# Performance work log

Hardware: AMD Instinct MI355X
Metric: run time of the kernel (lower is better)

The kernel has to match this reference:

```python
import jax, jax.numpy as jnp
import numpy as np

B, D, M, H = 512, 2048, 32, 64  # batch, d_model, memory_length, memory_hidden_dims

def _glu(x):
    a, b = jnp.split(x, 2, axis=-1)
    return a * jax.nn.sigmoid(b)

def setup_inputs() -> dict:
    key = jax.random.key(0)
    k1, k2, k3 = jax.random.split(key, 3)
    s1 = 1.0 / np.sqrt(M + 2 * H)
    s2 = 1.0 / np.sqrt(H + 2)
    return {
        "state_trace": jax.random.normal(k1, (B, D, M), jnp.float32),
        "w1a": jax.random.uniform(k2, (M, 2 * H, D), jnp.float32, -s1, s1),
        "b1a": jnp.zeros((1, D, 2 * H), jnp.float32),
        "Ta": jnp.ones((1,), jnp.float32),
        "w1b": jax.random.uniform(k3, (H, 2, D), jnp.float32, -s2, s2),
        "b1b": jnp.zeros((1, D, 2), jnp.float32),
        "Tb": jnp.ones((1,), jnp.float32),
    }

def reference(state_trace, w1a, b1a, Ta, w1b, b1b, Tb):
    # SuperLinear 1: per-feature grouped matmul over d_model (D axis)
    x = (jnp.einsum('BDM,MHD->BDH', state_trace, w1a) + b1a) / Ta  # [B, D, 2H]
    x = _glu(x)                                                     # [B, D, H]
    # SuperLinear 2
    x = (jnp.einsum('BDM,MHD->BDH', x, w1b) + b1b) / Tb             # [B, D, 2]
    x = _glu(x)                                                     # [B, D, 1]
    return x.squeeze(-1)                                            # [B, D]
```

## Files before the change

### kernel.cpp

```cpp
#include <hip/hip_runtime.h>
#include <hip/hip_bf16.h>


#define NB 512
#define ND 2048
#define NM 32
#define NH2 128
#define DCHUNK 8
#define BTILE 64

typedef __bf16 bf16x8 __attribute__((ext_vector_type(8)));
typedef __bf16 bf16x4 __attribute__((ext_vector_type(4)));
typedef float f32x4 __attribute__((ext_vector_type(4)));
typedef float f32x2 __attribute__((ext_vector_type(2)));

#define WSA_BYTES ((size_t)ND * NH2 * NM * 2)

__device__ __forceinline__ float sigmoid_fast(float x) {
    return __builtin_amdgcn_rcpf(1.0f + __builtin_amdgcn_exp2f(-1.442695040888963f * x));
}

__global__ __launch_bounds__(256) void transpose_w(const float* __restrict__ w1a,
                                                   const float* __restrict__ w1b,
                                                   __bf16* __restrict__ wsA,
                                                   float* __restrict__ wsB) {
    __shared__ float tile[64 * 65];
    const int tid = threadIdx.x;
    if (blockIdx.x < 2048) {
        const int h0 = (blockIdx.x & 63) * 2;
        const int d0 = (blockIdx.x >> 6) * 64;
        const int dc = tid & 63, wv = tid >> 6;
        #pragma unroll
        for (int k = 0; k < 16; ++k) {
            const int rr = wv + 4 * k;
            const int m = rr >> 1, hh = rr & 1;
            tile[rr * 65 + dc] = w1a[(size_t)(m * 128 + h0 + hh) * ND + d0 + dc];
        }
        __syncthreads();
        const int dloc = tid >> 2, seg = tid & 3;
        bf16x8 u0, u1;
        #pragma unroll
        for (int i = 0; i < 8; ++i) {
            const int q0 = seg * 16 + i;
            u0[i] = (__bf16)tile[((q0 & 31) * 2 + (q0 >> 5)) * 65 + dloc];
            const int q1 = seg * 16 + 8 + i;
            u1[i] = (__bf16)tile[((q1 & 31) * 2 + (q1 >> 5)) * 65 + dloc];
        }
        __bf16* dst = wsA + (size_t)(d0 + dloc) * (NH2 * NM) + h0 * 32 + seg * 16;
        *(bf16x8*)dst = u0;
        *(bf16x8*)(dst + 8) = u1;
    } else {
        const int d0 = (blockIdx.x - 2048) * 16;
        const int dcol = tid & 15, pr = tid >> 4;
        #pragma unroll
        for (int k = 0; k < 8; ++k) {
            const int p = pr + 16 * k;
            tile[p * 17 + dcol] = w1b[(size_t)p * ND + d0 + dcol];
        }
        __syncthreads();
        const int dloc = tid >> 4, j = tid & 15;
        #pragma unroll
        for (int i = 0; i < 8; ++i) {
            const int row = j * 8 + i;
            wsB[(size_t)(d0 + dloc) * 128 + j * 8 + i] = tile[row * 17 + dloc];
        }
    }
}

__global__ __launch_bounds__(256) void nlm_fused(
    const float*  __restrict__ st,
    const __bf16* __restrict__ wsA,
    const float*  __restrict__ b1a,
    const float*  __restrict__ Ta,
    const float*  __restrict__ wsB,
    const float*  __restrict__ b1b,
    const float*  __restrict__ Tb,
    float*        __restrict__ out)
{
    __shared__ __bf16 sst[BTILE][DCHUNK * NM + 4];
    __shared__ float  sout[BTILE][DCHUNK + 2];

    const int bid    = blockIdx.x;
    const int local  = bid >> 3;
    const int dchunk = (bid & 7) * 32 + (local & 31);
    const int btile  = local >> 5;
    const int d0 = dchunk * DCHUNK;
    const int b0 = btile * BTILE;

    const int tid  = threadIdx.x;
    const int wave = tid >> 6;
    const int lane = tid & 63;
    const int l15  = lane & 15;
    const int lg   = lane >> 4;

    {
        const float* base = st + (size_t)b0 * (ND * NM) + (size_t)d0 * NM;
        #pragma unroll
        for (int i = 0; i < 16; ++i) {
            const int idx = i * 256 + tid;
            const int b   = idx >> 6;
            const int off = (idx & 63) * 4;
            f32x4 v = *(const f32x4*)(base + (size_t)b * (ND * NM) + off);
            bf16x4 u;
            #pragma unroll
            for (int j = 0; j < 4; ++j) u[j] = (__bf16)v[j];
            *(bf16x4*)&sst[b][off] = u;
        }
    }
    __syncthreads();

    const float rTa = 1.0f / Ta[0];
    const float rTb = 1.0f / Tb[0];
    const int bloc = wave * 16 + l15;

    #pragma unroll
    for (int dd = 0; dd < DCHUNK; ++dd) {
        const int d = d0 + dd;

        const bf16x8 bfrag = *(const bf16x8*)&sst[bloc][dd * NM + lg * 8];

        const __bf16* wA = wsA + (size_t)d * (NH2 * NM);
        bf16x8 afrag[8];
        #pragma unroll
        for (int t = 0; t < 8; ++t)
            afrag[t] = *(const bf16x8*)(wA + (t * 16 + l15) * 32 + lg * 8);

        f32x4 acc[8];
        #pragma unroll
        for (int t = 0; t < 8; ++t)
            acc[t] = *(const f32x4*)(b1a + (size_t)d * 128 + t * 16 + lg * 4);
        #pragma unroll
        for (int t = 0; t < 8; ++t)
            acc[t] = __builtin_amdgcn_mfma_f32_16x16x32_bf16(afrag[t], bfrag, acc[t], 0, 0, 0);

        const float* w2d = wsB + (size_t)d * 128;
        float z0 = 0.0f, z1 = 0.0f;
        #pragma unroll
        for (int t = 0; t < 4; ++t) {
            const f32x4 wp0 = *(const f32x4*)(w2d + (t * 16 + lg * 4) * 2);
            const f32x4 wp1 = *(const f32x4*)(w2d + (t * 16 + lg * 4) * 2 + 4);
            #pragma unroll
            for (int r = 0; r < 4; ++r) {
                const float ya = acc[t][r]     * rTa;
                const float yb = acc[t + 4][r] * rTa;
                const float g  = ya * sigmoid_fast(yb);
                const float wa = (r < 2) ? wp0[2 * r]     : wp1[2 * (r - 2)];
                const float wb = (r < 2) ? wp0[2 * r + 1] : wp1[2 * (r - 2) + 1];
                z0 = fmaf(g, wa, z0);
                z1 = fmaf(g, wb, z1);
            }
        }
        z0 += __shfl_xor(z0, 16);
        z0 += __shfl_xor(z0, 32);
        z1 += __shfl_xor(z1, 16);
        z1 += __shfl_xor(z1, 32);
        if (lg == 0) {
            const float za = (z0 + b1b[d * 2 + 0]) * rTb;
            const float zb = (z1 + b1b[d * 2 + 1]) * rTb;
            sout[bloc][dd] = za * sigmoid_fast(zb);
        }
    }
    __syncthreads();

    if (tid < 128) {
        const int b = tid >> 1, q = (tid & 1) * 4;
        f32x4 v;
        #pragma unroll
        for (int j = 0; j < 4; ++j) v[j] = sout[b][q + j];
        *(f32x4*)(out + (size_t)(b0 + b) * ND + d0 + q) = v;
    }
}

extern "C" void kernel_launch(void* const* d_in, const int* in_sizes, int n_in,
                              void* d_out, int out_size, void* d_ws, size_t ws_size,
                              hipStream_t stream) {
    const float* st  = (const float*)d_in[0];
    const float* w1a = (const float*)d_in[1];
    const float* b1a = (const float*)d_in[2];
    const float* Ta  = (const float*)d_in[3];
    const float* w1b = (const float*)d_in[4];
    const float* b1b = (const float*)d_in[5];
    const float* Tb  = (const float*)d_in[6];
    float* out = (float*)d_out;

    __bf16* wsA = (__bf16*)d_ws;
    float*  wsB = (float*)((char*)d_ws + WSA_BYTES);

    transpose_w<<<dim3(2048 + 128), dim3(256), 0, stream>>>(w1a, w1b, wsA, wsB);
    nlm_fused<<<dim3(2048), dim3(256), 0, stream>>>(st, wsA, b1a, Ta, wsB, b1b, Tb, out);
}
```

Baseline: 268.9 us.

## Double-buffer weight fragments across d steps and batch state_trace loads

Issues all 16 state_trace global loads into registers before converting and storing them to LDS, so more memory requests are in flight at once. The per-d weight fragments are double-buffered: the next d's A fragments are prefetched while the current d's MFMAs and GLU epilogue run. The bias is moved out of the MFMA accumulator init into an FMA in the epilogue, and launch bounds request 3 blocks per CU. This aims to hide global load latency, at the cost of more registers, which may spill or lower occupancy.

New measurement: 267.2 us. Within noise of the previous version (-0.7%).

```diff
diff --git a/kernel.cpp b/kernel.cpp
--- a/kernel.cpp
+++ b/kernel.cpp
@@ -67,7 +67,7 @@
     }
 }
 
-__global__ __launch_bounds__(256) void nlm_fused(
+__global__ __launch_bounds__(256, 3) void nlm_fused(
     const float*  __restrict__ st,
     const __bf16* __restrict__ wsA,
     const float*  __restrict__ b1a,
@@ -93,45 +93,63 @@
     const int l15  = lane & 15;
     const int lg   = lane >> 4;
 
-    {
-        const float* base = st + (size_t)b0 * (ND * NM) + (size_t)d0 * NM;
-        #pragma unroll
-        for (int i = 0; i < 16; ++i) {
-            const int idx = i * 256 + tid;
-            const int b   = idx >> 6;
-            const int off = (idx & 63) * 4;
-            f32x4 v = *(const f32x4*)(base + (size_t)b * (ND * NM) + off);
-            bf16x4 u;
-            #pragma unroll
-            for (int j = 0; j < 4; ++j) u[j] = (__bf16)v[j];
-            *(bf16x4*)&sst[b][off] = u;
-        }
+    const float* base = st + (size_t)b0 * (ND * NM) + (size_t)d0 * NM;
+    f32x4 sv[16];
+    #pragma unroll
+    for (int i = 0; i < 16; ++i) {
+        const int idx = i * 256 + tid;
+        const int b   = idx >> 6;
+        const int off = (idx & 63) * 4;
+        sv[i] = *(const f32x4*)(base + (size_t)b * (ND * NM) + off);
+    }
+    #pragma unroll
+    for (int i = 0; i < 16; ++i) {
+        const int idx = i * 256 + tid;
+        const int b   = idx >> 6;
+        const int off = (idx & 63) * 4;
+        bf16x4 u;
+        #pragma unroll
+        for (int j = 0; j < 4; ++j) u[j] = (__bf16)sv[i][j];
+        *(bf16x4*)&sst[b][off] = u;
     }
     __syncthreads();
 
     const float rTa = 1.0f / Ta[0];
     const float rTb = 1.0f / Tb[0];
     const int bloc = wave * 16 + l15;
-
-    #pragma unroll
-    for (int dd = 0; dd < DCHUNK; ++dd) {
+    const size_t wstr = (size_t)(NH2 * NM);
+    const __bf16* wAl = wsA + l15 * 32 + lg * 8;
+
+    bf16x8 afA[8], afB[8];
+    {
+        const __bf16* p = wAl + (size_t)d0 * wstr;
+        #pragma unroll
+        for (int t = 0; t < 8; ++t) afA[t] = *(const bf16x8*)(p + t * 512);
+    }
+
+    auto step = [&](int dd, bf16x8 (&afC)[8], bf16x8 (&afN)[8]) {
         const int d = d0 + dd;
+        if (dd < 7) {
+            const __bf16* p = wAl + (size_t)(d + 1) * wstr;
+            #pragma unroll
+            for (int t = 0; t < 8; ++t) afN[t] = *(const bf16x8*)(p + t * 512);
+        }
+        f32x4 biP[8];
+        #pragma unroll
+        for (int t = 0; t < 8; ++t)
+            biP[t] = *(const f32x4*)(b1a + (size_t)d * 128 + t * 16 + lg * 4);
+        #pragma unroll
+        for (int t = 0; t < 8; ++t)
+            #pragma unroll
+            for (int r = 0; r < 4; ++r) biP[t][r] *= rTa;
 
         const bf16x8 bfrag = *(const bf16x8*)&sst[bloc][dd * NM + lg * 8];
-
-        const __bf16* wA = wsA + (size_t)d * (NH2 * NM);
-        bf16x8 afrag[8];
+        f32x4 acc[8];
+        #pragma unroll
+        for (int t = 0; t < 8; ++t) acc[t] = (f32x4){0.f, 0.f, 0.f, 0.f};
         #pragma unroll
         for (int t = 0; t < 8; ++t)
-            afrag[t] = *(const bf16x8*)(wA + (t * 16 + l15) * 32 + lg * 8);
-
-        f32x4 acc[8];
-        #pragma unroll
-        for (int t = 0; t < 8; ++t)
-            acc[t] = *(const f32x4*)(b1a + (size_t)d * 128 + t * 16 + lg * 4);
-        #pragma unroll
-        for (int t = 0; t < 8; ++t)
-            acc[t] = __builtin_amdgcn_mfma_f32_16x16x32_bf16(afrag[t], bfrag, acc[t], 0, 0, 0);
+            acc[t] = __builtin_amdgcn_mfma_f32_16x16x32_bf16(afC[t], bfrag, acc[t], 0, 0, 0);
 
         const float* w2d = wsB + (size_t)d * 128;
         float z0 = 0.0f, z1 = 0.0f;
@@ -141,8 +159,8 @@
             const f32x4 wp1 = *(const f32x4*)(w2d + (t * 16 + lg * 4) * 2 + 4);
             #pragma unroll
             for (int r = 0; r < 4; ++r) {
-                const float ya = acc[t][r]     * rTa;
-                const float yb = acc[t + 4][r] * rTa;
+                const float ya = fmaf(acc[t][r],     rTa, biP[t][r]);
+                const float yb = fmaf(acc[t + 4][r], rTa, biP[t + 4][r]);
                 const float g  = ya * sigmoid_fast(yb);
                 const float wa = (r < 2) ? wp0[2 * r]     : wp1[2 * (r - 2)];
                 const float wb = (r < 2) ? wp0[2 * r + 1] : wp1[2 * (r - 2) + 1];
@@ -159,7 +177,10 @@
             const float zb = (z1 + b1b[d * 2 + 1]) * rTb;
             sout[bloc][dd] = za * sigmoid_fast(zb);
         }
-    }
+    };
+    step(0, afA, afB); step(1, afB, afA); step(2, afA, afB); step(3, afB, afA);
+    step(4, afA, afB); step(5, afB, afA); step(6, afA, afB); step(7, afB, afA);
+
     __syncthreads();
 
     if (tid < 128) {
```
